# Optimization experiments

Hardware: AMD Instinct MI355X
Metric: run time of the kernel (lower is better)

## Reference

```python
import jax, jax.numpy as jnp
import numpy as np

# Quantization constants (mirror the torch module's __init__ kwargs)
INPUT_SCALE = 0.0625          # q_in: Quantize(input_scale, 0, qint8)
SCORE_SCALE = 0.00390625      # npu_matmul output_scale for scores (1/256)
PROB_SCALE = 0.00048828125    # q_probs: Quantize(prob_scale, 0, qint8) (1/2048)
I8_MIN, I8_MAX = -128, 127
I16_MIN, I16_MAX = -32768, 32767

D, K, M, N = 256, 256, 256, 65536  # w1:[K,D], x:[D,N], w2:[M,K]


def quantize_i8(x, scale):
    # torch Quantize: round-half-to-even(x/scale) + zp(=0), clamp to int8
    return jnp.clip(jnp.round(x / scale), I8_MIN, I8_MAX).astype(jnp.int8)


def npu_matmul_i16(w_i8, x_i8):
    acc = jnp.matmul(w_i8.astype(jnp.int32), x_i8.astype(jnp.int32))
    return jnp.clip(acc, I16_MIN, I16_MAX).astype(jnp.int16)


def setup_inputs() -> dict:
    key = jax.random.key(0)
    k1, k2, k3 = jax.random.split(key, 3)
    x = jax.random.normal(k1, (D, N), dtype=jnp.float32)
    # weights are pre-quantized int8 values stored as float32 (as in the torch module)
    w1 = jax.random.randint(k2, (K, D), -16, 16).astype(jnp.float32)
    w2 = jax.random.randint(k3, (M, K), -16, 16).astype(jnp.float32)
    return {"x": x, "w1": w1, "w2": w2}


def reference(x, w1, w2):
    x_q = quantize_i8(x, INPUT_SCALE)                       # [D, N] int8
    scores_q = npu_matmul_i16(w1.astype(jnp.int8), x_q)     # [K, N] int16 (quantized, scale=SCORE_SCALE)
    scores = scores_q.astype(jnp.float32) * SCORE_SCALE     # dequantize
    probs = jax.nn.softmax(scores, axis=0)                  # softmax over dim 0
    q_probs = quantize_i8(probs, PROB_SCALE)                # [K, N] int8
    out = npu_matmul_i16(w2.astype(jnp.int8), q_probs)      # [M, N] int16
    return out
```

## Files before the change

kernel.cpp:

```cpp
#include <hip/hip_runtime.h>

typedef int   int4v   __attribute__((ext_vector_type(4)));
typedef float float4v __attribute__((ext_vector_type(4)));

#define N_DIM 65536

__device__ __forceinline__ int quant8(float v) {
    int q = (int)rintf(v);
    q = q > 127 ? 127 : q;
    q = q < -128 ? -128 : q;
    return q;
}

__device__ __forceinline__ int clamp16(int s) {
    s = s > 32767 ? 32767 : s;
    s = s < -32768 ? -32768 : s;
    return s;
}

__device__ __forceinline__ unsigned int qpack(float4v v) {
    int q0 = quant8(v.x * 16.0f);
    int q1 = quant8(v.y * 16.0f);
    int q2 = quant8(v.z * 16.0f);
    int q3 = quant8(v.w * 16.0f);
    return (unsigned int)((q0 & 0xff) | ((q1 & 0xff) << 8) |
                          ((q2 & 0xff) << 16) | ((q3 & 0xff) << 24));
}

__device__ __forceinline__ float fexp2(float a) {
    float r;
    asm("v_exp_f32 %0, %1" : "=v"(r) : "v"(a));
    return r;
}

__global__ __launch_bounds__(256) void quant_weights(const float* __restrict__ w1,
                                                     const float* __restrict__ w2,
                                                     unsigned char* __restrict__ w1q,
                                                     unsigned char* __restrict__ w2q) {
    int idx = blockIdx.x * 256 + threadIdx.x;
    const float* src;
    unsigned char* dst;
    int off;
    if (idx < 16384) { src = w1; dst = w1q; off = idx * 4; }
    else             { src = w2; dst = w2q; off = (idx - 16384) * 4; }
    float4v f = *reinterpret_cast<const float4v*>(src + off);
    unsigned int dw = (unsigned int)(((int)f.x & 0xff) | (((int)f.y & 0xff) << 8) |
                                     (((int)f.z & 0xff) << 16) | (((int)f.w & 0xff) << 24));
    *reinterpret_cast<unsigned int*>(dst + off) = dw;
}

__global__ __launch_bounds__(512, 3) void qdq_main(const float* __restrict__ x,
                                                   const unsigned char* __restrict__ w1q,
                                                   const unsigned char* __restrict__ w2q,
                                                   int* __restrict__ out) {
    __shared__ unsigned char xq[8192];
    __shared__ unsigned char pq[8192];
    __shared__ int   mb[8][32];
    __shared__ float sb[8][32];

    const int tid  = threadIdx.x;
    const int wv   = tid >> 6;
    const int lane = tid & 63;
    const int c    = lane & 15;
    const int g    = lane >> 4;

    const int rsub = lane >> 3;
    const int cg   = lane & 7;
    const int R    = rsub & 3;
    const unsigned int sel1 = (R & 1) ? 0x03070206u : 0x05010400u;
    const unsigned int sel2 = (R & 2) ? 0x07060302u : 0x01000504u;
    const int colsel = (0x3120 >> (R * 4)) & 0xF;
    const int n_t = cg * 4 + colsel;
    const int qb  = rsub & 4;

    int4v a1f[2][4];
    {
        const unsigned char* a1 = w1q + (size_t)(wv * 32 + c) * 256 + g * 16;
        #pragma unroll
        for (int rt = 0; rt < 2; ++rt)
            #pragma unroll
            for (int kk = 0; kk < 4; ++kk)
                a1f[rt][kk] = *reinterpret_cast<const int4v*>(a1 + rt * 4096 + kk * 64);
    }
    const unsigned char* a2 = w2q + (size_t)(wv * 32 + c) * 256 + g * 16;

    const int colstart = blockIdx.x * 128;
    const float* xpb = x + (size_t)(wv * 32 + rsub) * N_DIM + cg * 4;

    float4v raw[4];
    #pragma unroll
    for (int i = 0; i < 4; ++i)
        raw[i] = *reinterpret_cast<const float4v*>(xpb + (size_t)i * (8 * N_DIM) + colstart);

    const float C = 0.0056355275034725134f;

    for (int it = 0; it < 4; ++it) {
        const int col0 = colstart + it * 32;

        unsigned int Wq[4];
        #pragma unroll
        for (int i = 0; i < 4; ++i) Wq[i] = qpack(raw[i]);
        if (it < 3) {
            #pragma unroll
            for (int i = 0; i < 4; ++i)
                raw[i] = *reinterpret_cast<const float4v*>(
                    xpb + (size_t)i * (8 * N_DIM) + (col0 + 32));
        }

        #pragma unroll
        for (int i = 0; i < 4; ++i) {
            unsigned int t = (unsigned int)__shfl_xor((int)Wq[i], 8);
            unsigned int Q = __builtin_amdgcn_perm(t, Wq[i], sel1);
            unsigned int u = (unsigned int)__shfl_xor((int)Q, 16);
            unsigned int F = __builtin_amdgcn_perm(Q, u, sel2);
            const int dbase = wv * 32 + i * 8 + qb;
            *reinterpret_cast<unsigned int*>(
                xq + n_t * 256 + (dbase ^ ((n_t & 15) << 4))) = F;
        }
        __syncthreads();

        int4v bq[2][4];
        #pragma unroll
        for (int t2 = 0; t2 < 2; ++t2)
            #pragma unroll
            for (int kk = 0; kk < 4; ++kk)
                bq[t2][kk] = *reinterpret_cast<const int4v*>(
                    xq + (t2 * 16 + c) * 256 + ((kk * 64 + g * 16) ^ (c << 4)));

        unsigned int scA[4], scB[4];
        int imA = -(1 << 30), imB = -(1 << 30);
        #pragma unroll
        for (int rt = 0; rt < 2; ++rt) {
            int4v accA = {0, 0, 0, 0}, accB = {0, 0, 0, 0};
            #pragma unroll
            for (int kk = 0; kk < 4; ++kk) {
                accA = __builtin_amdgcn_mfma_i32_16x16x64_i8(a1f[rt][kk], bq[0][kk], accA, 0, 0, 0);
                accB = __builtin_amdgcn_mfma_i32_16x16x64_i8(a1f[rt][kk], bq[1][kk], accB, 0, 0, 0);
            }
            {
                const int s0 = clamp16(accA[0]), s1 = clamp16(accA[1]);
                const int s2 = clamp16(accA[2]), s3 = clamp16(accA[3]);
                int m01 = s0 > s1 ? s0 : s1, m23 = s2 > s3 ? s2 : s3;
                int m = m01 > m23 ? m01 : m23;
                imA = imA > m ? imA : m;
                scA[2 * rt]     = (unsigned int)((s0 & 0xffff) | (s1 << 16));
                scA[2 * rt + 1] = (unsigned int)((s2 & 0xffff) | (s3 << 16));
            }
            {
                const int s0 = clamp16(accB[0]), s1 = clamp16(accB[1]);
                const int s2 = clamp16(accB[2]), s3 = clamp16(accB[3]);
                int m01 = s0 > s1 ? s0 : s1, m23 = s2 > s3 ? s2 : s3;
                int m = m01 > m23 ? m01 : m23;
                imB = imB > m ? imB : m;
                scB[2 * rt]     = (unsigned int)((s0 & 0xffff) | (s1 << 16));
                scB[2 * rt + 1] = (unsigned int)((s2 & 0xffff) | (s3 << 16));
            }
        }

        {
            int o = __shfl_xor(imA, 16); imA = imA > o ? imA : o;
            o = __shfl_xor(imA, 32);     imA = imA > o ? imA : o;
            o = __shfl_xor(imB, 16);     imB = imB > o ? imB : o;
            o = __shfl_xor(imB, 32);     imB = imB > o ? imB : o;
        }
        if (g == 0) mb[wv][c] = imA;
        else if (g == 1) mb[wv][16 + c] = imB;
        float eA[8], eB[8];
        float sA = 0.0f, sB = 0.0f;
        #pragma unroll
        for (int i = 0; i < 4; ++i) {
            eA[2 * i]     = fexp2((float)((int)(short)(scA[i] & 0xffffu) - imA) * C);
            eA[2 * i + 1] = fexp2((float)(((int)scA[i] >> 16) - imA) * C);
            sA += eA[2 * i] + eA[2 * i + 1];
            eB[2 * i]     = fexp2((float)((int)(short)(scB[i] & 0xffffu) - imB) * C);
            eB[2 * i + 1] = fexp2((float)(((int)scB[i] >> 16) - imB) * C);
            sB += eB[2 * i] + eB[2 * i + 1];
        }
        sA += __shfl_xor(sA, 16); sA += __shfl_xor(sA, 32);
        sB += __shfl_xor(sB, 16); sB += __shfl_xor(sB, 32);
        if (g == 0) sb[wv][c] = sA;
        else if (g == 1) sb[wv][16 + c] = sB;

        int4v a2f[2][4];
        #pragma unroll
        for (int rt = 0; rt < 2; ++rt)
            #pragma unroll
            for (int kk = 0; kk < 4; ++kk)
                a2f[rt][kk] = *reinterpret_cast<const int4v*>(a2 + rt * 4096 + kk * 64);
        __syncthreads();

        int gmA = -(1 << 30), gmB = -(1 << 30);
        #pragma unroll
        for (int j = 0; j < 8; ++j) {
            int a = mb[j][c], b = mb[j][16 + c];
            gmA = gmA > a ? gmA : a;
            gmB = gmB > b ? gmB : b;
        }
        float gsA = 0.0f, gsB = 0.0f;
        #pragma unroll
        for (int j = 0; j < 8; ++j) {
            gsA += sb[j][c]      * fexp2((float)(mb[j][c] - gmA) * C);
            gsB += sb[j][16 + c] * fexp2((float)(mb[j][16 + c] - gmB) * C);
        }
        const float qsA = (2048.0f / gsA) * fexp2((float)(imA - gmA) * C);
        const float qsB = (2048.0f / gsB) * fexp2((float)(imB - gmB) * C);

        #pragma unroll
        for (int rt = 0; rt < 2; ++rt) {
            const int koff = wv * 32 + rt * 16 + g * 4;
            {
                int q0 = (int)rintf(eA[4 * rt + 0] * qsA);
                int q1 = (int)rintf(eA[4 * rt + 1] * qsA);
                int q2 = (int)rintf(eA[4 * rt + 2] * qsA);
                int q3 = (int)rintf(eA[4 * rt + 3] * qsA);
                q0 = q0 > 127 ? 127 : q0;
                q1 = q1 > 127 ? 127 : q1;
                q2 = q2 > 127 ? 127 : q2;
                q3 = q3 > 127 ? 127 : q3;
                *reinterpret_cast<unsigned int*>(
                    pq + c * 256 + (koff ^ (c << 4))) =
                    (unsigned int)(q0 | (q1 << 8) | (q2 << 16) | (q3 << 24));
            }
            {
                int q0 = (int)rintf(eB[4 * rt + 0] * qsB);
                int q1 = (int)rintf(eB[4 * rt + 1] * qsB);
                int q2 = (int)rintf(eB[4 * rt + 2] * qsB);
                int q3 = (int)rintf(eB[4 * rt + 3] * qsB);
                q0 = q0 > 127 ? 127 : q0;
                q1 = q1 > 127 ? 127 : q1;
                q2 = q2 > 127 ? 127 : q2;
                q3 = q3 > 127 ? 127 : q3;
                *reinterpret_cast<unsigned int*>(
                    pq + (16 + c) * 256 + (koff ^ (c << 4))) =
                    (unsigned int)(q0 | (q1 << 8) | (q2 << 16) | (q3 << 24));
            }
        }
        __syncthreads();

        int4v b2[2][4];
        #pragma unroll
        for (int t2 = 0; t2 < 2; ++t2)
            #pragma unroll
            for (int kk = 0; kk < 4; ++kk)
                b2[t2][kk] = *reinterpret_cast<const int4v*>(
                    pq + (t2 * 16 + c) * 256 + ((kk * 64 + g * 16) ^ (c << 4)));

        #pragma unroll
        for (int rt = 0; rt < 2; ++rt) {
            int4v accA = {0, 0, 0, 0}, accB = {0, 0, 0, 0};
            #pragma unroll
            for (int kk = 0; kk < 4; ++kk) {
                accA = __builtin_amdgcn_mfma_i32_16x16x64_i8(a2f[rt][kk], b2[0][kk], accA, 0, 0, 0);
                accB = __builtin_amdgcn_mfma_i32_16x16x64_i8(a2f[rt][kk], b2[1][kk], accB, 0, 0, 0);
            }
            #pragma unroll
            for (int r = 0; r < 4; ++r) {
                const size_t rowoff =
                    (size_t)(wv * 32 + rt * 16 + g * 4 + r) * N_DIM + col0;
                __builtin_nontemporal_store(clamp16(accA[r]), &out[rowoff + c]);
                __builtin_nontemporal_store(clamp16(accB[r]), &out[rowoff + 16 + c]);
            }
        }
    }
}

extern "C" void kernel_launch(void* const* d_in, const int* in_sizes, int n_in,
                              void* d_out, int out_size, void* d_ws, size_t ws_size,
                              hipStream_t stream) {
    const float* x  = (const float*)d_in[0];
    const float* w1 = (const float*)d_in[1];
    const float* w2 = (const float*)d_in[2];
    int* out = (int*)d_out;

    unsigned char* w1q = (unsigned char*)d_ws;
    unsigned char* w2q = w1q + 65536;

    quant_weights<<<128, 256, 0, stream>>>(w1, w2, w1q, w2q);
    qdq_main<<<512, 512, 0, stream>>>(x, w1q, w2q, out);
}
```

Measured before the change: 46.73 us.

## Split fused kernel into softmax phase and second-matmul phase via global buffer

Splits the fused kernel into two launches. The first computes the first matmul and softmax and writes the quantized probabilities to a global workspace buffer (16 MB of int8). The second kernel reads them back and performs the second matmul plus output stores. This frees LDS and registers and removes a barrier per iteration, but adds a full global round trip of the probability matrix and an extra kernel launch.

```diff
diff --git a/kernel.cpp b/kernel.cpp
--- a/kernel.cpp
+++ b/kernel.cpp
@@ -49,12 +49,10 @@
     *reinterpret_cast<unsigned int*>(dst + off) = dw;
 }
 
-__global__ __launch_bounds__(512, 3) void qdq_main(const float* __restrict__ x,
-                                                   const unsigned char* __restrict__ w1q,
-                                                   const unsigned char* __restrict__ w2q,
-                                                   int* __restrict__ out) {
+__global__ __launch_bounds__(512, 3) void qdq_phase1(const float* __restrict__ x,
+                                                     const unsigned char* __restrict__ w1q,
+                                                     unsigned char* __restrict__ pqg) {
     __shared__ unsigned char xq[8192];
-    __shared__ unsigned char pq[8192];
     __shared__ int   mb[8][32];
     __shared__ float sb[8][32];
 
@@ -82,7 +80,6 @@
             for (int kk = 0; kk < 4; ++kk)
                 a1f[rt][kk] = *reinterpret_cast<const int4v*>(a1 + rt * 4096 + kk * 64);
     }
-    const unsigned char* a2 = w2q + (size_t)(wv * 32 + c) * 256 + g * 16;
 
     const int colstart = blockIdx.x * 128;
     const float* xpb = x + (size_t)(wv * 32 + rsub) * N_DIM + cg * 4;
@@ -180,13 +177,6 @@
         sB += __shfl_xor(sB, 16); sB += __shfl_xor(sB, 32);
         if (g == 0) sb[wv][c] = sA;
         else if (g == 1) sb[wv][16 + c] = sB;
-
-        int4v a2f[2][4];
-        #pragma unroll
-        for (int rt = 0; rt < 2; ++rt)
-            #pragma unroll
-            for (int kk = 0; kk < 4; ++kk)
-                a2f[rt][kk] = *reinterpret_cast<const int4v*>(a2 + rt * 4096 + kk * 64);
         __syncthreads();
 
         int gmA = -(1 << 30), gmB = -(1 << 30);
@@ -218,7 +208,7 @@
                 q2 = q2 > 127 ? 127 : q2;
                 q3 = q3 > 127 ? 127 : q3;
                 *reinterpret_cast<unsigned int*>(
-                    pq + c * 256 + (koff ^ (c << 4))) =
+                    pqg + (size_t)(col0 + c) * 256 + (koff ^ (c << 4))) =
                     (unsigned int)(q0 | (q1 << 8) | (q2 << 16) | (q3 << 24));
             }
             {
@@ -231,11 +221,37 @@
                 q2 = q2 > 127 ? 127 : q2;
                 q3 = q3 > 127 ? 127 : q3;
                 *reinterpret_cast<unsigned int*>(
-                    pq + (16 + c) * 256 + (koff ^ (c << 4))) =
+                    pqg + (size_t)(col0 + 16 + c) * 256 + (koff ^ (c << 4))) =
                     (unsigned int)(q0 | (q1 << 8) | (q2 << 16) | (q3 << 24));
             }
         }
-        __syncthreads();
+    }
+}
+
+__global__ __launch_bounds__(512) void qdq_phase2(const unsigned char* __restrict__ pqg,
+                                                  const unsigned char* __restrict__ w2q,
+                                                  int* __restrict__ out) {
+    const int tid  = threadIdx.x;
+    const int wv   = tid >> 6;
+    const int lane = tid & 63;
+    const int c    = lane & 15;
+    const int g    = lane >> 4;
+
+    int4v a2f[2][4];
+    {
+        const unsigned char* a2 = w2q + (size_t)(wv * 32 + c) * 256 + g * 16;
+        #pragma unroll
+        for (int rt = 0; rt < 2; ++rt)
+            #pragma unroll
+            for (int kk = 0; kk < 4; ++kk)
+                a2f[rt][kk] = *reinterpret_cast<const int4v*>(a2 + rt * 4096 + kk * 64);
+    }
+
+    const int colstart = blockIdx.x * 128;
+
+    #pragma unroll
+    for (int it = 0; it < 4; ++it) {
+        const int col0 = colstart + it * 32;
 
         int4v b2[2][4];
         #pragma unroll
@@ -243,7 +259,8 @@
             #pragma unroll
             for (int kk = 0; kk < 4; ++kk)
                 b2[t2][kk] = *reinterpret_cast<const int4v*>(
-                    pq + (t2 * 16 + c) * 256 + ((kk * 64 + g * 16) ^ (c << 4)));
+                    pqg + (size_t)(col0 + t2 * 16 + c) * 256 +
+                    ((kk * 64 + g * 16) ^ (c << 4)));
 
         #pragma unroll
         for (int rt = 0; rt < 2; ++rt) {
@@ -274,7 +291,9 @@
 
     unsigned char* w1q = (unsigned char*)d_ws;
     unsigned char* w2q = w1q + 65536;
+    unsigned char* pqg = w2q + 65536;
 
     quant_weights<<<128, 256, 0, stream>>>(w1, w2, w1q, w2q);
-    qdq_main<<<512, 512, 0, stream>>>(x, w1q, w2q, out);
-}
+    qdq_phase1<<<512, 512, 0, stream>>>(x, w1q, pqg);
+    qdq_phase2<<<512, 512, 0, stream>>>(pqg, w2q, out);
+}
```

After: 51.97 us. 1.11x slower.
